# Performance work log

Measured on AMD Instinct MI355X. Metric: run time of the kernel, lower is better.

The kernel has to match this reference:

```python
import jax, jax.numpy as jnp
import numpy as np

B, N, D = 4, 512, 256  # batch, num_diseases, feature_dim == hidden_dim
H = 256                # hidden_dim
EPS = 1e-5

def _layernorm(x, g, b):
    m = jnp.mean(x, axis=-1, keepdims=True)
    v = jnp.mean((x - m) ** 2, axis=-1, keepdims=True)
    return (x - m) * jax.lax.rsqrt(v + EPS) * g + b

def setup_inputs() -> dict:
    key = jax.random.key(0)
    ks = jax.random.split(key, 16)
    s = 0.02
    return {
        "x": jax.random.normal(ks[0], (B, N, D), jnp.float32),
        "area_matrix": jax.random.uniform(ks[1], (B, N), jnp.float32),
        "co_occurrence": jax.random.uniform(ks[2], (N, N), jnp.float32),
        "Wq": jax.random.normal(ks[3], (H, D), jnp.float32) * s,
        "bq": jnp.zeros((H,), jnp.float32),
        "Wk": jax.random.normal(ks[4], (H, D), jnp.float32) * s,
        "bk": jnp.zeros((H,), jnp.float32),
        "Wv": jax.random.normal(ks[5], (H, D), jnp.float32) * s,
        "bv": jnp.zeros((H,), jnp.float32),
        "We1": jax.random.normal(ks[6], (H, 2), jnp.float32) * 0.5,
        "be1": jnp.zeros((H,), jnp.float32),
        "We2": jax.random.normal(ks[7], (1, H), jnp.float32) * s,
        "be2": jnp.zeros((1,), jnp.float32),
        "Wo": jax.random.normal(ks[8], (H, H), jnp.float32) * s,
        "bo": jnp.zeros((H,), jnp.float32),
        "g_ot": jnp.ones((H,), jnp.float32),
        "b_ot": jnp.zeros((H,), jnp.float32),
        "g1": jnp.ones((H,), jnp.float32),
        "b1": jnp.zeros((H,), jnp.float32),
        "g2": jnp.ones((H,), jnp.float32),
        "b2": jnp.zeros((H,), jnp.float32),
    }

def reference(x, area_matrix, co_occurrence, Wq, bq, Wk, bk, Wv, bv,
              We1, be1, We2, be2, Wo, bo, g_ot, b_ot, g1, b1, g2, b2):
    # projections: (B, N, H)
    q = jnp.einsum('bnd,hd->bnh', x, Wq) + bq
    k = jnp.einsum('bnd,hd->bnh', x, Wk) + bk
    v = jnp.einsum('bnd,hd->bnh', x, Wv) + bv
    attn_scores = jnp.einsum('bih,bjh->bij', q, k) / jnp.sqrt(jnp.float32(H))
    # edge inputs: (B, N, N, 2) = stack(broadcast area along last N, broadcast co-occ along batch)
    area = jnp.broadcast_to(area_matrix[:, :, None], (B, N, N))
    co = jnp.broadcast_to(co_occurrence[None], (B, N, N))
    edge_inputs = jnp.stack([area, co], axis=-1)
    h = jax.nn.relu(jnp.einsum('bije,he->bijh', edge_inputs, We1) + be1)
    edge_weights = jax.nn.sigmoid(jnp.einsum('bijh,oh->bijo', h, We2) + be2)[..., 0]
    attn_probs = jax.nn.softmax(attn_scores * edge_weights, axis=-1)  # dropout = identity (eval)
    out = jnp.einsum('bij,bjh->bih', attn_probs, v)
    out = _layernorm(out, g1, b1)
    out = jax.nn.relu(_layernorm(jnp.einsum('bnh,oh->bno', out, Wo) + bo, g_ot, b_ot))
    out = _layernorm(out + x, g2, b2)
    return out
```

## Files before the change

kernel.cpp:

```cpp
#include <hip/hip_runtime.h>

typedef unsigned short u16;
typedef unsigned int u32;

#define NB 4
#define NN 512
#define ND 256
#define NH 256
#define TI 4

typedef __attribute__((ext_vector_type(8))) short short8;
typedef __attribute__((ext_vector_type(4))) float f32x4;

__device__ __forceinline__ short bf(float f) {
    u32 t; __builtin_memcpy(&t, &f, 4);
    u32 r = (t + 0x7FFFu + ((t >> 16) & 1u)) >> 16;
    return (short)(u16)r;
}

__device__ __forceinline__ float waveReduceSum(float v) {
#pragma unroll
    for (int o = 32; o > 0; o >>= 1) v += __shfl_down(v, o);
    return v;
}

__device__ __forceinline__ float4 blockReduce4(float4 v, float4* red4b, bool ismax) {
#pragma unroll
    for (int o = 32; o > 0; o >>= 1) {
        float4 t;
        t.x = __shfl_down(v.x, o); t.y = __shfl_down(v.y, o);
        t.z = __shfl_down(v.z, o); t.w = __shfl_down(v.w, o);
        if (ismax) {
            v.x = fmaxf(v.x, t.x); v.y = fmaxf(v.y, t.y);
            v.z = fmaxf(v.z, t.z); v.w = fmaxf(v.w, t.w);
        } else {
            v.x += t.x; v.y += t.y; v.z += t.z; v.w += t.w;
        }
    }
    int wid = threadIdx.x >> 6;
    __syncthreads();
    if ((threadIdx.x & 63) == 0) red4b[wid] = v;
    __syncthreads();
    float4 r = red4b[0];
#pragma unroll
    for (int w = 1; w < 8; ++w) {
        float4 u = red4b[w];
        if (ismax) {
            r.x = fmaxf(r.x, u.x); r.y = fmaxf(r.y, u.y);
            r.z = fmaxf(r.z, u.z); r.w = fmaxf(r.w, u.w);
        } else {
            r.x += u.x; r.y += u.y; r.z += u.z; r.w += u.w;
        }
    }
    return r;
}

__global__ __launch_bounds__(256) void qkv_mfma(
    const float* __restrict__ x,
    const float* __restrict__ Wq, const float* __restrict__ bq,
    const float* __restrict__ Wk, const float* __restrict__ bk,
    const float* __restrict__ Wv, const float* __restrict__ bv,
    const float* __restrict__ Wo,
    float* __restrict__ q, float* __restrict__ k_t, float* __restrict__ v,
    float* __restrict__ Wot)
{
    const int tid = threadIdx.x;
    if (blockIdx.y == 48) {
        __shared__ float t[32][33];
        const int tx = tid & 31, ty = tid >> 5;
#pragma unroll
        for (int tt2 = 0; tt2 < 2; ++tt2) {
            const int tile = blockIdx.x * 2 + tt2;
            const int bx = tile & 7, by = tile >> 3;
            __syncthreads();
#pragma unroll
            for (int k = 0; k < 4; ++k)
                t[ty + 8 * k][tx] = Wo[(size_t)(by * 32 + ty + 8 * k) * 256 + bx * 32 + tx];
            __syncthreads();
#pragma unroll
            for (int k = 0; k < 4; ++k)
                Wot[(size_t)(bx * 32 + ty + 8 * k) * 256 + by * 32 + tx] = t[tx][ty + 8 * k];
        }
        return;
    }

    const int lane = tid & 63, wave = tid >> 6;
    const int r0 = blockIdx.x * 64 + wave * 16;
    const int out0 = blockIdx.y * 16;
    const int which = blockIdx.y >> 4;
    const float* W   = (which == 0) ? Wq : (which == 1) ? Wk : Wv;
    const float* bia = (which == 0) ? bq : (which == 1) ? bk : bv;

    const int m = lane & 15, koff = (lane >> 4) * 8;
    const float* Ap = x + (size_t)(r0 + m) * 256 + koff;
    const float* Bp = W + (size_t)((out0 & 255) + m) * 256 + koff;

    f32x4 acc = {0.f, 0.f, 0.f, 0.f};
#pragma unroll
    for (int kb = 0; kb < 8; ++kb) {
        float4 a0 = *(const float4*)(Ap + kb * 32);
        float4 a1 = *(const float4*)(Ap + kb * 32 + 4);
        float4 b0 = *(const float4*)(Bp + kb * 32);
        float4 b1 = *(const float4*)(Bp + kb * 32 + 4);
        short8 af, bf8;
        af[0] = bf(a0.x); af[1] = bf(a0.y); af[2] = bf(a0.z); af[3] = bf(a0.w);
        af[4] = bf(a1.x); af[5] = bf(a1.y); af[6] = bf(a1.z); af[7] = bf(a1.w);
        bf8[0] = bf(b0.x); bf8[1] = bf(b0.y); bf8[2] = bf(b0.z); bf8[3] = bf(b0.w);
        bf8[4] = bf(b1.x); bf8[5] = bf(b1.y); bf8[6] = bf(b1.z); bf8[7] = bf(b1.w);
        acc = __builtin_amdgcn_mfma_f32_16x16x32_bf16(af, bf8, acc, 0, 0, 0);
    }

    const int oc = (out0 + m) & 255;
    const float bias = bia[oc];
    const int rbase = r0 + (lane >> 4) * 4;
#pragma unroll
    for (int reg = 0; reg < 4; ++reg) {
        int R = rbase + reg;
        float val = acc[reg] + bias;
        if (which == 1)      k_t[((size_t)(R >> 9) * 256 + oc) * 512 + (R & 511)] = val;
        else if (which == 0) q[(size_t)R * 256 + oc] = val;
        else                 v[(size_t)R * 256 + oc] = val;
    }
}

__global__ __launch_bounds__(512) void fused_kernel(
    const float* __restrict__ x, const float* __restrict__ area, const float* __restrict__ co,
    const float* __restrict__ We1, const float* __restrict__ be1,
    const float* __restrict__ We2, const float* __restrict__ be2,
    const float* __restrict__ Wot, const float* __restrict__ bo,
    const float* __restrict__ g_ot, const float* __restrict__ b_ot,
    const float* __restrict__ g1, const float* __restrict__ b1,
    const float* __restrict__ g2, const float* __restrict__ b2,
    const float* __restrict__ q, const float* __restrict__ k_t, const float* __restrict__ v,
    float* __restrict__ out)
{
    const int tid = threadIdx.x;
    const int b = blockIdx.x >> 7;
    const int i0 = (blockIdx.x & 127) << 2;
    const int lane = tid & 63, w = tid >> 6;

    __shared__ float histS[1024], histB[1024], hist2S[1024], hist2B[1024];
    __shared__ float srow[2048];
    __shared__ float4 red4b[8];
    __shared__ float sBaseS[4], sBaseB[4], redA[8], redB[8];

    const float be2f = be2[0];

    histS[tid] = 0.f; histS[tid + 512] = 0.f;
    histB[tid] = 0.f; histB[tid + 512] = 0.f;
    __syncthreads();
    {
        const int s = tid >> 7, h0 = tid & 127;
        const float a = area[b * NN + i0 + s];
        float baS = 0.f, baB = 0.f;
#pragma unroll
        for (int k = 0; k < 2; ++k) {
            const int h = h0 + 128 * k;
            const float w10 = We1[2 * h], w11 = We1[2 * h + 1];
            const float w2v = We2[h], be1v = be1[h];
            const float al = fmaf(a, w10, be1v);
            const float sl = w11 * w2v, bb = al * w2v;
            if (w11 == 0.f) {
                if (al > 0.f) baB += bb;
            } else {
                float tt = -al / w11;
                if (w11 > 0.f) {
                    if (tt <= 0.f)      { baS += sl; baB += bb; }
                    else if (tt < 1.f) {
                        int u = (int)(tt * 256.f); u = u > 255 ? 255 : u;
                        atomicAdd(&histS[s * 256 + u], sl);
                        atomicAdd(&histB[s * 256 + u], bb);
                    }
                } else {
                    if (tt >= 1.f)      { baS += sl; baB += bb; }
                    else if (tt > 0.f) {
                        baS += sl; baB += bb;
                        int u = (int)(tt * 256.f); u = u > 255 ? 255 : u;
                        atomicAdd(&histS[s * 256 + u], -sl);
                        atomicAdd(&histB[s * 256 + u], -bb);
                    }
                }
            }
        }
        float rS = waveReduceSum(baS), rB = waveReduceSum(baB);
        if (lane == 0) { redA[w] = rS; redB[w] = rB; }
    }
    __syncthreads();
    if (tid < 4) {
        sBaseS[tid] = redA[2 * tid] + redA[2 * tid + 1];
        sBaseB[tid] = redB[2 * tid] + redB[2 * tid + 1];
    }

    {
        float* sa = histS; float* sb = histB; float* da = hist2S; float* db = hist2B;
        const int col = tid & 255;
        const int s2 = (tid >> 8) * 2;
        for (int off = 1; off < 256; off <<= 1) {
            const int i1 = s2 * 256 + col, i2 = (s2 + 1) * 256 + col;
            float v1a = sa[i1], v1b = sb[i1], v2a = sa[i2], v2b = sb[i2];
            if (col >= off) {
                v1a += sa[i1 - off]; v1b += sb[i1 - off];
                v2a += sa[i2 - off]; v2b += sb[i2 - off];
            }
            da[i1] = v1a; db[i1] = v1b; da[i2] = v2a; db[i2] = v2b;
            __syncthreads();
            float* t = sa; sa = da; da = t;
            t = sb; sb = db; db = t;
        }
    }

    float sA[TI];
    {
        const float* kt = k_t + (size_t)b * NH * NN + tid;
        const float* qb_ = q + (size_t)(b * NN + i0) * NH;
        float dot[TI] = {0.f, 0.f, 0.f, 0.f};
        for (int h = 0; h < 256; h += 4) {
            float k0 = kt[(size_t)(h + 0) * 512];
            float k1 = kt[(size_t)(h + 1) * 512];
            float k2 = kt[(size_t)(h + 2) * 512];
            float k3 = kt[(size_t)(h + 3) * 512];
#pragma unroll
            for (int ti = 0; ti < TI; ++ti) {
                float4 qv = *(const float4*)&qb_[ti * 256 + h];
                dot[ti] += qv.x * k0 + qv.y * k1 + qv.z * k2 + qv.w * k3;
            }
        }
#pragma unroll
        for (int ti = 0; ti < TI; ++ti) {
            float c = co[(size_t)(i0 + ti) * NN + tid];
            int u = (int)(c * 256.f); u = u > 255 ? 255 : u;
            float S = sBaseS[ti] + histS[ti * 256 + u];
            float B = sBaseB[ti] + histB[ti * 256 + u];
            float e = fmaf(c, S, B) + be2f;
            float ew = 1.f / (1.f + __expf(-e));
            sA[ti] = dot[ti] * 0.0625f * ew;
        }
    }

    {
        float4 m4 = make_float4(sA[0], sA[1], sA[2], sA[3]);
        m4 = blockReduce4(m4, red4b, true);
        float eA[TI];
        float4 s4;
#pragma unroll
        for (int ti = 0; ti < TI; ++ti) {
            eA[ti] = __expf(sA[ti] - ((const float*)&m4)[ti]);
            ((float*)&s4)[ti] = eA[ti];
        }
        s4 = blockReduce4(s4, red4b, false);
#pragma unroll
        for (int ti = 0; ti < TI; ++ti)
            srow[ti * 512 + tid] = eA[ti] * (1.f / ((const float*)&s4)[ti]);
        __syncthreads();
    }

    const int hP = tid & 255, half = tid >> 8;
    float accv[TI] = {0.f, 0.f, 0.f, 0.f};
    {
        const float* vp = v + (size_t)b * NN * NH + hP;
        for (int j4 = half * 64; j4 < half * 64 + 64; ++j4) {
            const int jj = 4 * j4;
            float v0 = vp[(size_t)(jj + 0) * NH];
            float v1 = vp[(size_t)(jj + 1) * NH];
            float v2 = vp[(size_t)(jj + 2) * NH];
            float v3 = vp[(size_t)(jj + 3) * NH];
#pragma unroll
            for (int ti = 0; ti < TI; ++ti) {
                float4 p4 = *(const float4*)&srow[ti * 512 + jj];
                accv[ti] += p4.x * v0 + p4.y * v1 + p4.z * v2 + p4.w * v3;
            }
        }
        if (half == 1) {
#pragma unroll
            for (int ti = 0; ti < TI; ++ti) hist2S[ti * 256 + hP] = accv[ti];
        }
        __syncthreads();
        if (half == 0) {
#pragma unroll
            for (int ti = 0; ti < TI; ++ti) accv[ti] += hist2S[ti * 256 + hP];
        }
    }

    float4 t4;
    float dd[TI];
#pragma unroll
    for (int ti = 0; ti < TI; ++ti) ((float*)&t4)[ti] = (half == 0) ? accv[ti] : 0.f;
    float4 mean4 = blockReduce4(t4, red4b, false);
#pragma unroll
    for (int ti = 0; ti < TI; ++ti) {
        dd[ti] = (half == 0) ? accv[ti] - ((const float*)&mean4)[ti] * (1.f / 256.f) : 0.f;
        ((float*)&t4)[ti] = dd[ti] * dd[ti];
    }
    float4 var4 = blockReduce4(t4, red4b, false);
    if (half == 0) {
        const float g1v = g1[hP], b1v = b1[hP];
#pragma unroll
        for (int ti = 0; ti < TI; ++ti)
            srow[ti * 256 + hP] = dd[ti] * rsqrtf(((const float*)&var4)[ti] * (1.f / 256.f) + 1e-5f) * g1v + b1v;
    }
    __syncthreads();

    float acc2[TI] = {0.f, 0.f, 0.f, 0.f};
    {
        for (int d4 = half * 32; d4 < half * 32 + 32; ++d4) {
            const int d = 4 * d4;
            float w0 = Wot[(size_t)(d + 0) * 256 + hP];
            float w1 = Wot[(size_t)(d + 1) * 256 + hP];
            float w2c = Wot[(size_t)(d + 2) * 256 + hP];
            float w3 = Wot[(size_t)(d + 3) * 256 + hP];
#pragma unroll
            for (int ti = 0; ti < TI; ++ti) {
                float4 y4 = *(const float4*)&srow[ti * 256 + d];
                acc2[ti] += y4.x * w0 + y4.y * w1 + y4.z * w2c + y4.w * w3;
            }
        }
        if (half == 1) {
#pragma unroll
            for (int ti = 0; ti < TI; ++ti) histS[ti * 256 + hP] = acc2[ti];
        }
        __syncthreads();
        if (half == 0) {
            const float bov = bo[hP];
#pragma unroll
            for (int ti = 0; ti < TI; ++ti) acc2[ti] += histS[ti * 256 + hP] + bov;
        }
    }

#pragma unroll
    for (int ti = 0; ti < TI; ++ti) ((float*)&t4)[ti] = (half == 0) ? acc2[ti] : 0.f;
    mean4 = blockReduce4(t4, red4b, false);
#pragma unroll
    for (int ti = 0; ti < TI; ++ti) {
        dd[ti] = (half == 0) ? acc2[ti] - ((const float*)&mean4)[ti] * (1.f / 256.f) : 0.f;
        ((float*)&t4)[ti] = dd[ti] * dd[ti];
    }
    var4 = blockReduce4(t4, red4b, false);
    float z[TI];
    const float gotv = (half == 0) ? g_ot[hP] : 0.f;
    const float botv = (half == 0) ? b_ot[hP] : 0.f;
#pragma unroll
    for (int ti = 0; ti < TI; ++ti)
        z[ti] = fmaxf(dd[ti] * rsqrtf(((const float*)&var4)[ti] * (1.f / 256.f) + 1e-5f) * gotv + botv, 0.f);

    float tt[TI];
#pragma unroll
    for (int ti = 0; ti < TI; ++ti) {
        tt[ti] = (half == 0) ? z[ti] + x[(size_t)(b * NN + i0 + ti) * ND + hP] : 0.f;
        ((float*)&t4)[ti] = tt[ti];
    }
    mean4 = blockReduce4(t4, red4b, false);
#pragma unroll
    for (int ti = 0; ti < TI; ++ti) {
        dd[ti] = (half == 0) ? tt[ti] - ((const float*)&mean4)[ti] * (1.f / 256.f) : 0.f;
        ((float*)&t4)[ti] = dd[ti] * dd[ti];
    }
    var4 = blockReduce4(t4, red4b, false);
    if (half == 0) {
        const float g2v = g2[hP], b2v = b2[hP];
#pragma unroll
        for (int ti = 0; ti < TI; ++ti) {
            float o = dd[ti] * rsqrtf(((const float*)&var4)[ti] * (1.f / 256.f) + 1e-5f) * g2v + b2v;
            out[(size_t)(b * NN + i0 + ti) * NH + hP] = o;
        }
    }
}

extern "C" void kernel_launch(void* const* d_in, const int* in_sizes, int n_in,
                              void* d_out, int out_size, void* d_ws, size_t ws_size,
                              hipStream_t stream) {
    const float* x    = (const float*)d_in[0];
    const float* area = (const float*)d_in[1];
    const float* co   = (const float*)d_in[2];
    const float* Wq   = (const float*)d_in[3];
    const float* bq   = (const float*)d_in[4];
    const float* Wk   = (const float*)d_in[5];
    const float* bk   = (const float*)d_in[6];
    const float* Wv   = (const float*)d_in[7];
    const float* bv   = (const float*)d_in[8];
    const float* We1  = (const float*)d_in[9];
    const float* be1  = (const float*)d_in[10];
    const float* We2  = (const float*)d_in[11];
    const float* be2  = (const float*)d_in[12];
    const float* Wo   = (const float*)d_in[13];
    const float* bo   = (const float*)d_in[14];
    const float* g_ot = (const float*)d_in[15];
    const float* b_ot = (const float*)d_in[16];
    const float* g1   = (const float*)d_in[17];
    const float* b1   = (const float*)d_in[18];
    const float* g2   = (const float*)d_in[19];
    const float* b2   = (const float*)d_in[20];

    float* q   = (float*)d_ws;
    float* k_t = q + (size_t)NB * NN * NH;
    float* v   = k_t + (size_t)NB * NN * NH;
    float* Wot = v + (size_t)NB * NN * NH;

    qkv_mfma<<<dim3(32, 49), 256, 0, stream>>>(x, Wq, bq, Wk, bk, Wv, bv, Wo,
                                               q, k_t, v, Wot);
    fused_kernel<<<NB * NN / TI, 512, 0, stream>>>(x, area, co, We1, be1, We2, be2, Wot, bo,
                                                   g_ot, b_ot, g1, b1, g2, b2, q, k_t, v,
                                                   (float*)d_out);
}
```

Before: 172.0 us.

## Store K, V and transposed Wo as packed bf16 pairs to halve load traffic

The projection kernel now writes K, V and the transposed Wo as bf16, packed so that two adjacent hidden channels share one 32-bit word, while Q stays fp32. The fused kernel reads these packed words and unpacks them with shifts, and the P·V loop is split four ways across the block with partial sums combined in shared memory. The goal is to halve the global/L2 bytes streamed by every block in the score, PV and output-projection loops. The cost is extra bf16 rounding of K, V and Wo, plus more shared-memory reduction work.

Result: faster. 168.1 us (-2.3%).

```diff
diff --git a/kernel.cpp b/kernel.cpp
--- a/kernel.cpp
+++ b/kernel.cpp
@@ -16,6 +16,12 @@
     u32 t; __builtin_memcpy(&t, &f, 4);
     u32 r = (t + 0x7FFFu + ((t >> 16) & 1u)) >> 16;
     return (short)(u16)r;
+}
+__device__ __forceinline__ float blo(u32 u) {
+    u32 t = u << 16; float f; __builtin_memcpy(&f, &t, 4); return f;
+}
+__device__ __forceinline__ float bhi(u32 u) {
+    u32 t = u & 0xFFFF0000u; float f; __builtin_memcpy(&f, &t, 4); return f;
 }
 
 __device__ __forceinline__ float waveReduceSum(float v) {
@@ -61,8 +67,8 @@
     const float* __restrict__ Wk, const float* __restrict__ bk,
     const float* __restrict__ Wv, const float* __restrict__ bv,
     const float* __restrict__ Wo,
-    float* __restrict__ q, float* __restrict__ k_t, float* __restrict__ v,
-    float* __restrict__ Wot)
+    float* __restrict__ q, u16* __restrict__ kp, u16* __restrict__ vp,
+    u16* __restrict__ wop)
 {
     const int tid = threadIdx.x;
     if (blockIdx.y == 48) {
@@ -78,8 +84,10 @@
                 t[ty + 8 * k][tx] = Wo[(size_t)(by * 32 + ty + 8 * k) * 256 + bx * 32 + tx];
             __syncthreads();
 #pragma unroll
-            for (int k = 0; k < 4; ++k)
-                Wot[(size_t)(bx * 32 + ty + 8 * k) * 256 + by * 32 + tx] = t[tx][ty + 8 * k];
+            for (int k = 0; k < 4; ++k) {
+                const int d = bx * 32 + ty + 8 * k, o = by * 32 + tx;
+                wop[(size_t)(d >> 1) * 512 + 2 * o + (d & 1)] = (u16)bf(t[tx][ty + 8 * k]);
+            }
         }
         return;
     }
@@ -117,9 +125,14 @@
     for (int reg = 0; reg < 4; ++reg) {
         int R = rbase + reg;
         float val = acc[reg] + bias;
-        if (which == 1)      k_t[((size_t)(R >> 9) * 256 + oc) * 512 + (R & 511)] = val;
-        else if (which == 0) q[(size_t)R * 256 + oc] = val;
-        else                 v[(size_t)R * 256 + oc] = val;
+        if (which == 0) {
+            q[(size_t)R * 256 + oc] = val;
+        } else if (which == 1) {
+            const int b_ = R >> 9, n = R & 511;
+            kp[((size_t)(b_ * 128 + (oc >> 1)) * 512 + n) * 2 + (oc & 1)] = (u16)bf(val);
+        } else {
+            vp[(size_t)R * 256 + oc] = (u16)bf(val);
+        }
     }
 }
 
@@ -127,11 +140,11 @@
     const float* __restrict__ x, const float* __restrict__ area, const float* __restrict__ co,
     const float* __restrict__ We1, const float* __restrict__ be1,
     const float* __restrict__ We2, const float* __restrict__ be2,
-    const float* __restrict__ Wot, const float* __restrict__ bo,
+    const u32* __restrict__ wop32, const float* __restrict__ bo,
     const float* __restrict__ g_ot, const float* __restrict__ b_ot,
     const float* __restrict__ g1, const float* __restrict__ b1,
     const float* __restrict__ g2, const float* __restrict__ b2,
-    const float* __restrict__ q, const float* __restrict__ k_t, const float* __restrict__ v,
+    const float* __restrict__ q, const u32* __restrict__ kp32, const u32* __restrict__ vp32,
     float* __restrict__ out)
 {
     const int tid = threadIdx.x;
@@ -211,14 +224,14 @@
 
     float sA[TI];
     {
-        const float* kt = k_t + (size_t)b * NH * NN + tid;
+        const u32* kt = kp32 + (size_t)b * 128 * 512 + tid;
         const float* qb_ = q + (size_t)(b * NN + i0) * NH;
         float dot[TI] = {0.f, 0.f, 0.f, 0.f};
         for (int h = 0; h < 256; h += 4) {
-            float k0 = kt[(size_t)(h + 0) * 512];
-            float k1 = kt[(size_t)(h + 1) * 512];
-            float k2 = kt[(size_t)(h + 2) * 512];
-            float k3 = kt[(size_t)(h + 3) * 512];
+            const int h2 = h >> 1;
+            u32 ka = kt[(size_t)h2 * 512];
+            u32 kb = kt[(size_t)(h2 + 1) * 512];
+            float k0 = blo(ka), k1 = bhi(ka), k2 = blo(kb), k3 = bhi(kb);
 #pragma unroll
             for (int ti = 0; ti < TI; ++ti) {
                 float4 qv = *(const float4*)&qb_[ti * 256 + h];
@@ -254,31 +267,40 @@
         __syncthreads();
     }
 
+    {
+        const int h2 = tid & 127, qtr = tid >> 7;
+        float a0[TI] = {0.f, 0.f, 0.f, 0.f};
+        float a1[TI] = {0.f, 0.f, 0.f, 0.f};
+        const u32* vp_ = vp32 + (size_t)b * 512 * 128 + h2;
+        const float4* s4p = (const float4*)srow;
+        for (int j4 = qtr * 32; j4 < qtr * 32 + 32; ++j4) {
+            const int jj = 4 * j4;
+            u32 va = vp_[(size_t)(jj + 0) * 128];
+            u32 vb = vp_[(size_t)(jj + 1) * 128];
+            u32 vc = vp_[(size_t)(jj + 2) * 128];
+            u32 vd = vp_[(size_t)(jj + 3) * 128];
+            float la = blo(va), ha = bhi(va), lb = blo(vb), hb = bhi(vb);
+            float lc = blo(vc), hc = bhi(vc), ld = blo(vd), hd = bhi(vd);
+#pragma unroll
+            for (int ti = 0; ti < TI; ++ti) {
+                float4 p4 = s4p[ti * 128 + j4];
+                a0[ti] += p4.x * la + p4.y * lb + p4.z * lc + p4.w * ld;
+                a1[ti] += p4.x * ha + p4.y * hb + p4.z * hc + p4.w * hd;
+            }
+        }
+        float2* bq_ = (float2*)((qtr == 0) ? histS : (qtr == 1) ? histB : (qtr == 2) ? hist2S : hist2B);
+#pragma unroll
+        for (int ti = 0; ti < TI; ++ti) bq_[ti * 128 + h2] = make_float2(a0[ti], a1[ti]);
+        __syncthreads();
+    }
+
     const int hP = tid & 255, half = tid >> 8;
     float accv[TI] = {0.f, 0.f, 0.f, 0.f};
-    {
-        const float* vp = v + (size_t)b * NN * NH + hP;
-        for (int j4 = half * 64; j4 < half * 64 + 64; ++j4) {
-            const int jj = 4 * j4;
-            float v0 = vp[(size_t)(jj + 0) * NH];
-            float v1 = vp[(size_t)(jj + 1) * NH];
-            float v2 = vp[(size_t)(jj + 2) * NH];
-            float v3 = vp[(size_t)(jj + 3) * NH];
-#pragma unroll
-            for (int ti = 0; ti < TI; ++ti) {
-                float4 p4 = *(const float4*)&srow[ti * 512 + jj];
-                accv[ti] += p4.x * v0 + p4.y * v1 + p4.z * v2 + p4.w * v3;
-            }
-        }
-        if (half == 1) {
-#pragma unroll
-            for (int ti = 0; ti < TI; ++ti) hist2S[ti * 256 + hP] = accv[ti];
-        }
-        __syncthreads();
-        if (half == 0) {
-#pragma unroll
-            for (int ti = 0; ti < TI; ++ti) accv[ti] += hist2S[ti * 256 + hP];
-        }
+    if (half == 0) {
+#pragma unroll
+        for (int ti = 0; ti < TI; ++ti)
+            accv[ti] = histS[ti * 256 + hP] + histB[ti * 256 + hP]
+                     + hist2S[ti * 256 + hP] + hist2B[ti * 256 + hP];
     }
 
     float4 t4;
@@ -302,16 +324,22 @@
 
     float acc2[TI] = {0.f, 0.f, 0.f, 0.f};
     {
-        for (int d4 = half * 32; d4 < half * 32 + 32; ++d4) {
-            const int d = 4 * d4;
-            float w0 = Wot[(size_t)(d + 0) * 256 + hP];
-            float w1 = Wot[(size_t)(d + 1) * 256 + hP];
-            float w2c = Wot[(size_t)(d + 2) * 256 + hP];
-            float w3 = Wot[(size_t)(d + 3) * 256 + hP];
+        const u32* wp = wop32 + hP;
+        const float4* y4p = (const float4*)srow;
+        for (int d8 = half * 16; d8 < half * 16 + 16; ++d8) {
+            const int d2 = 4 * d8;
+            u32 w01 = wp[(size_t)(d2 + 0) * 256];
+            u32 w23 = wp[(size_t)(d2 + 1) * 256];
+            u32 w45 = wp[(size_t)(d2 + 2) * 256];
+            u32 w67 = wp[(size_t)(d2 + 3) * 256];
+            float f0 = blo(w01), f1 = bhi(w01), f2 = blo(w23), f3 = bhi(w23);
+            float f4 = blo(w45), f5 = bhi(w45), f6 = blo(w67), f7 = bhi(w67);
 #pragma unroll
             for (int ti = 0; ti < TI; ++ti) {
-                float4 y4 = *(const float4*)&srow[ti * 256 + d];
-                acc2[ti] += y4.x * w0 + y4.y * w1 + y4.z * w2c + y4.w * w3;
+                float4 ya = y4p[ti * 64 + 2 * d8];
+                float4 yb = y4p[ti * 64 + 2 * d8 + 1];
+                acc2[ti] += ya.x * f0 + ya.y * f1 + ya.z * f2 + ya.w * f3
+                          + yb.x * f4 + yb.y * f5 + yb.z * f6 + yb.w * f7;
             }
         }
         if (half == 1) {
@@ -390,14 +418,16 @@
     const float* g2   = (const float*)d_in[19];
     const float* b2   = (const float*)d_in[20];
 
-    float* q   = (float*)d_ws;
-    float* k_t = q + (size_t)NB * NN * NH;
-    float* v   = k_t + (size_t)NB * NN * NH;
-    float* Wot = v + (size_t)NB * NN * NH;
+    float* q  = (float*)d_ws;
+    u16*  kp  = (u16*)(q + (size_t)2048 * 256);
+    u16*  vp  = kp + (size_t)4 * 128 * 512 * 2;
+    u16*  wop = vp + (size_t)2048 * 256;
 
     qkv_mfma<<<dim3(32, 49), 256, 0, stream>>>(x, Wq, bq, Wk, bk, Wv, bv, Wo,
-                                               q, k_t, v, Wot);
-    fused_kernel<<<NB * NN / TI, 512, 0, stream>>>(x, area, co, We1, be1, We2, be2, Wot, bo,
-                                                   g_ot, b_ot, g1, b1, g2, b2, q, k_t, v,
+                                               q, kp, vp, wop);
+    fused_kernel<<<NB * NN / TI, 512, 0, stream>>>(x, area, co, We1, be1, We2, be2,
+                                                   (const u32*)wop, bo,
+                                                   g_ot, b_ot, g1, b1, g2, b2,
+                                                   q, (const u32*)kp, (const u32*)vp,
                                                    (float*)d_out);
 }
```
